# Optimization experiments

Measured on AMD Instinct MI355X. Metric: run time of the kernel, lower is better.

## Reference

```python
import jax, jax.numpy as jnp
import numpy as np

# Config (matches init_kwargs): GRU decoder, score_model='default',
# local_att='False', context_vector_concat='True'. Dropout layers are
# identity (Keras eager call defaults to training=False).
B, L, FEAT = 256, 64, 2048   # batch, attention locations, feature channels
UNITS, EMB, VOCAB = 512, 256, 32000


def setup_inputs() -> dict:
    key = jax.random.key(0)
    ks = jax.random.split(key, 16)
    s = 0.02
    inp = {
        "x_tokens": jax.random.randint(ks[0], (B, 1), 0, VOCAB),
        "features": jax.random.normal(ks[1], (B, L, FEAT), jnp.float32),
        "hidden": jax.random.normal(ks[2], (B, UNITS), jnp.float32),
        # attention params
        "W1": jax.random.normal(ks[3], (FEAT, UNITS), jnp.float32) * s,
        "b1": jnp.zeros((UNITS,), jnp.float32),
        "W2": jax.random.normal(ks[4], (UNITS, UNITS), jnp.float32) * s,
        "b2": jnp.zeros((UNITS,), jnp.float32),
        "V": jax.random.normal(ks[5], (UNITS, 1), jnp.float32) * s,
        "bV": jnp.zeros((1,), jnp.float32),
        "W3": jax.random.normal(ks[6], (FEAT + UNITS, UNITS), jnp.float32) * s,
        "b3": jnp.zeros((UNITS,), jnp.float32),
        # embedding
        "emb_table": jax.random.normal(ks[7], (VOCAB, EMB), jnp.float32) * s,
        # GRU params (gate order z, r, h), input dim = UNITS + EMB
        "gru_kernel": jax.random.normal(ks[8], (UNITS + EMB, 3 * UNITS), jnp.float32) * s,
        "gru_rec": jax.random.normal(ks[9], (UNITS, 3 * UNITS), jnp.float32) * s,
        "gru_bias": jnp.zeros((3 * UNITS,), jnp.float32),
        # output heads
        "fc1_W": jax.random.normal(ks[10], (UNITS, UNITS), jnp.float32) * s,
        "fc1_b": jnp.zeros((UNITS,), jnp.float32),
        "fc2_W": jax.random.normal(ks[11], (UNITS, VOCAB), jnp.float32) * s,
        "fc2_b": jnp.zeros((VOCAB,), jnp.float32),
    }
    return inp


def _gru_step(x_t, h_prev, kernel, rec, bias):
    # Keras GRU single step (reset_after=False), gate order z, r, h.
    u = UNITS
    gx = x_t @ kernel + bias                       # [B, 3u]
    gh = h_prev @ rec                              # [B, 3u]
    z = jax.nn.sigmoid(gx[:, :u] + gh[:, :u])
    r = jax.nn.sigmoid(gx[:, u:2 * u] + gh[:, u:2 * u])
    hh = jnp.tanh(gx[:, 2 * u:] + r * gh[:, 2 * u:])
    return z * h_prev + (1.0 - z) * hh


def reference(x_tokens, features, hidden, W1, b1, W2, b2, V, bV, W3, b3,
              emb_table, gru_kernel, gru_rec, gru_bias,
              fc1_W, fc1_b, fc2_W, fc2_b):
    # Bahdanau attention, score_model='default'
    score = jnp.tanh(features @ W1 + b1 + (hidden @ W2 + b2)[:, None, :])  # [B,L,U]
    logits = score @ V + bV                                               # [B,L,1]
    attn = jax.nn.softmax(logits, axis=1)                                 # [B,L,1]
    context = jnp.sum(attn * features, axis=1)                            # [B,FEAT]
    # context_vector_concat == 'True'
    cvh = jnp.tanh(jnp.concatenate([context, hidden], axis=-1)) @ W3 + b3  # [B,U]
    # embedding + concat with context (seq len 1)
    emb = emb_table[x_tokens]                                             # [B,1,E]
    x_in = jnp.concatenate([cvh[:, None, :], emb], axis=-1)               # [B,1,U+E]
    # GRU over length-1 sequence; Keras Sequential uses zero initial state
    h0 = jnp.zeros((x_in.shape[0], UNITS), x_in.dtype)
    h_new = _gru_step(x_in[:, 0, :], h0, gru_kernel, gru_rec, gru_bias)   # [B,U]
    out = h_new[:, None, :]                                               # [B,1,U]
    x1 = out @ fc1_W + fc1_b                                              # [B,1,U]
    x1 = x1.reshape(-1, x1.shape[2])                                      # [B,U]
    logits_out = x1 @ fc2_W + fc2_b                                       # [B,VOCAB]
    return logits_out, h_new, attn
```

## Files before the change

kernel.cpp:

```cpp
#include <hip/hip_runtime.h>
#include <hip/hip_bf16.h>

#define B_N 256
#define L_Q 64
#define FEAT_N 2048
#define UNITS_N 512
#define EMB_N 256
#define VOCAB_N 32000

typedef __attribute__((ext_vector_type(8))) short bf16x8;
typedef __attribute__((ext_vector_type(4))) float f32x4;

__device__ __forceinline__ unsigned short f2bf(float x) {
  union { float f; unsigned int u; } c; c.f = x;
  unsigned int u = c.u + 0x7FFFu + ((c.u >> 16) & 1u);
  return (unsigned short)(u >> 16);
}

__device__ __forceinline__ float sigmoidf_(float x) { return 1.0f / (1.0f + __expf(-x)); }

__device__ __forceinline__ void store_frag4(unsigned short* base, int KS, int row, int k0,
                                            float a, float b, float c, float d) {
  int rt = row >> 4, lr = row & 15;
  int ks = k0 >> 5, lq = (k0 >> 3) & 3, j0 = k0 & 7;
  union { unsigned long long u; unsigned short s[4]; } p;
  p.s[0] = f2bf(a); p.s[1] = f2bf(b); p.s[2] = f2bf(c); p.s[3] = f2bf(d);
  *reinterpret_cast<unsigned long long*>(base + (((rt * KS + ks) * 64) + (lq * 16 + lr)) * 8 + j0) = p.u;
}

__device__ __forceinline__ void gload_lds16(const void* g, void* lds) {
  __builtin_amdgcn_global_load_lds(
      (const __attribute__((address_space(1))) unsigned int*)(uintptr_t)g,
      (__attribute__((address_space(3))) unsigned int*)(unsigned)(uintptr_t)lds,
      16, 0, 0);
}

__device__ __forceinline__ void wfrag_one(const float* __restrict__ W, int N, int KS,
                                          unsigned short* __restrict__ dst, int tid, int gruMap) {
  int l = tid & 63;
  int ks = (tid >> 6) % KS;
  int cts = tid / (64 * KS);
  int ct = cts & 3, nt = cts >> 2;
  int nb = gruMap ? (nt < 8 ? nt * 64 : 1024 + (nt - 8) * 64) : nt * 64;
  int ncol = nb + ct * 16 + (l & 15);
  int k0 = ks * 32 + (l >> 4) * 8;
  union { bf16x8 v; unsigned short s[8]; } fr;
#pragma unroll
  for (int j = 0; j < 8; ++j) fr.s[j] = f2bf(W[(size_t)(k0 + j) * N + ncol]);
  *reinterpret_cast<bf16x8*>(dst + (size_t)tid * 8) = fr.v;
}

__global__ void k_prep_all(const float* __restrict__ W1, unsigned short* __restrict__ W1s,
                           const float* __restrict__ hidden,
                           const float* __restrict__ emb_table,
                           const int* __restrict__ tok,
                           unsigned short* __restrict__ hfrag,
                           unsigned short* __restrict__ xinfrag,
                           const float* __restrict__ W2, unsigned short* __restrict__ W2f,
                           const float* __restrict__ W3, unsigned short* __restrict__ W3f,
                           const float* __restrict__ gruK, unsigned short* __restrict__ gruf,
                           const float* __restrict__ fc1W, unsigned short* __restrict__ fc1f) {
  int bb = blockIdx.x;
  if (bb < 512) {
    int t = bb * 256 + threadIdx.x;
    int l = t & 63;
    int c = (t >> 6) & 31;
    int kt = t >> 11;
    int n = c * 16 + (l & 15);
    int k0 = kt * 32 + (l >> 4) * 8;
    union { bf16x8 v; unsigned short s[8]; } fr;
#pragma unroll
    for (int j = 0; j < 8; ++j) fr.s[j] = f2bf(W1[(size_t)(k0 + j) * UNITS_N + n]);
    *reinterpret_cast<bf16x8*>(W1s + (size_t)t * 8) = fr.v;
  } else if (bb < 704) {
    int t = (bb - 512) * 256 + threadIdx.x;
    if (t < 32768) {
      int b = t >> 7, k0 = (t & 127) * 4;
      const float* s = hidden + (size_t)b * UNITS_N + k0;
      store_frag4(hfrag, 16, b, k0, s[0], s[1], s[2], s[3]);
    } else if (t < 49152) {
      int t2 = t - 32768;
      int b = t2 >> 6, e0 = (t2 & 63) * 4;
      const float* s = emb_table + (size_t)tok[b] * EMB_N + e0;
      store_frag4(xinfrag, 24, b, 512 + e0, s[0], s[1], s[2], s[3]);
    }
  } else if (bb < 832) {
    wfrag_one(W2, 512, 16, W2f, (bb - 704) * 256 + threadIdx.x, 0);
  } else if (bb < 1472) {
    wfrag_one(W3, 512, 80, W3f, (bb - 832) * 256 + threadIdx.x, 0);
  } else if (bb < 1856) {
    wfrag_one(gruK, 1536, 24, gruf, (bb - 1472) * 256 + threadIdx.x, 1);
  } else {
    wfrag_one(fc1W, 512, 16, fc1f, (bb - 1856) * 256 + threadIdx.x, 0);
  }
}

template <int MODE>
__launch_bounds__(256)
__global__ void k_small2(const unsigned short* __restrict__ Afrag, int KS,
                         const unsigned short* __restrict__ Bfrag,
                         const float* __restrict__ bias,
                         float* __restrict__ outF, int N,
                         unsigned short* __restrict__ outFrag, int KSo) {
  constexpr int NCT = (MODE == 2) ? 8 : 4;
  __shared__ f32x4 red[4][2][NCT][64];
  int t = threadIdx.x, w = t >> 6, l = t & 63;
  int nt = blockIdx.x;
  int mb = blockIdx.y;
  int KSq = KS >> 2;

  f32x4 acc[2][NCT];
#pragma unroll
  for (int rt = 0; rt < 2; ++rt)
#pragma unroll
    for (int ct = 0; ct < NCT; ++ct) acc[rt][ct] = (f32x4){0.f, 0.f, 0.f, 0.f};

  for (int s = 0; s < KSq; ++s) {
    int ks = w * KSq + s;
    bf16x8 af[2];
#pragma unroll
    for (int rt = 0; rt < 2; ++rt)
      af[rt] = *reinterpret_cast<const bf16x8*>(Afrag + (((size_t)(mb * 2 + rt) * KS + ks) * 64 + l) * 8);
#pragma unroll
    for (int ct = 0; ct < NCT; ++ct) {
      int tile = (MODE == 2) ? (ct < 4 ? nt : 8 + nt) : nt;
      int cts = ct & 3;
      bf16x8 bf = *reinterpret_cast<const bf16x8*>(Bfrag + (((size_t)(tile * 4 + cts) * KS + ks) * 64 + l) * 8);
#pragma unroll
      for (int rt = 0; rt < 2; ++rt)
        acc[rt][ct] = __builtin_amdgcn_mfma_f32_16x16x32_bf16(af[rt], bf, acc[rt][ct], 0, 0, 0);
    }
  }

#pragma unroll
  for (int rt = 0; rt < 2; ++rt)
#pragma unroll
    for (int ct = 0; ct < NCT; ++ct) red[w][rt][ct][l] = acc[rt][ct];
  __syncthreads();

#pragma unroll
  for (int si = 0; si < 2; ++si) {
    int s = t + si * 256;
    int l2 = s & 63, ct = (s >> 6) & 3, rt = s >> 8;
    f32x4 v = red[0][rt][ct][l2];
#pragma unroll
    for (int ww = 1; ww < 4; ++ww) v += red[ww][rt][ct][l2];
    int col = nt * 64 + ct * 16 + (l2 & 15);
    int row0 = mb * 32 + rt * 16 + (l2 >> 4) * 4;
    if (MODE == 2) {
      f32x4 vh = red[0][rt][ct + 4][l2];
#pragma unroll
      for (int ww = 1; ww < 4; ++ww) vh += red[ww][rt][ct + 4][l2];
      float bz = bias[col], bh = bias[1024 + col];
#pragma unroll
      for (int i = 0; i < 4; ++i) {
        float hv = (1.f - sigmoidf_(v[i] + bz)) * tanhf(vh[i] + bh);
        int row = row0 + i;
        outF[(size_t)row * UNITS_N + col] = hv;
        int k = col;
        outFrag[(((size_t)(row >> 4) * KSo + (k >> 5)) * 64 + (((k >> 3) & 3) * 16 + (row & 15))) * 8 + (k & 7)] = f2bf(hv);
      }
    } else {
      float bv = bias[col];
#pragma unroll
      for (int i = 0; i < 4; ++i) {
        float vv = v[i] + bv;
        int row = row0 + i;
        if (MODE == 0) {
          outF[(size_t)row * N + col] = vv;
        } else {
          int k = col;
          outFrag[(((size_t)(row >> 4) * KSo + (k >> 5)) * 64 + (((k >> 3) & 3) * 16 + (row & 15))) * 8 + (k & 7)] = f2bf(vv);
        }
      }
    }
  }
}


#define G7_LOADA(S0, S1, KF)                                       \
  { const float* p_ = Ap + (size_t)(KF) * 32;                      \
    S0 = *reinterpret_cast<const float4*>(p_);                     \
    S1 = *reinterpret_cast<const float4*>(p_ + 4); }

#define G7_STAGEB(KF, BUF)                                                          \
  { _Pragma("unroll")                                                               \
    for (int i_ = 0; i_ < 4; ++i_) {                                                \
      int s_ = w * 4 + i_;                                                          \
      gload_lds16(W1c + ((size_t)((KF) * 32 + h * 16 + s_) << 10) + (size_t)l * 16, \
                  BbC + (size_t)(BUF) * 16384 + (s_ << 10));                        \
    } }

#define G7_CONVA(S0, S1, BUF)                                      \
  { union { bf16x8 v; unsigned short s8[8]; } u_;                  \
    u_.s8[0] = f2bf(S0.x); u_.s8[1] = f2bf(S0.y);                  \
    u_.s8[2] = f2bf(S0.z); u_.s8[3] = f2bf(S0.w);                  \
    u_.s8[4] = f2bf(S1.x); u_.s8[5] = f2bf(S1.y);                  \
    u_.s8[6] = f2bf(S1.z); u_.s8[7] = f2bf(S1.w);                  \
    *reinterpret_cast<bf16x8*>(&Ab[BUF][awi]) = u_.v; }

#define G7_BODY(KT, L0, L1, C0, C1)                                           \
  { const int kt_ = (KT);                                                     \
    if (kt_ + 2 < 64) G7_LOADA(L0, L1, kt_ + 2);                              \
    if (kt_ + 1 < 64) {                                                       \
      G7_STAGEB(kt_ + 1, (kt_ + 1) & 1);                                      \
      G7_CONVA(C0, C1, (kt_ + 1) & 1);                                        \
    }                                                                         \
    bf16x8 af_[4];                                                            \
    _Pragma("unroll")                                                         \
    for (int rt_ = 0; rt_ < 4; ++rt_)                                         \
      af_[rt_] = *reinterpret_cast<const bf16x8*>(                            \
          &Ab[kt_ & 1][((rt_ * 4 + (l >> 4)) * 16 + (l & 15)) * 8]);          \
    _Pragma("unroll")                                                         \
    for (int ct_ = 0; ct_ < 4; ++ct_) {                                       \
      bf16x8 bfr_ = *reinterpret_cast<const bf16x8*>(                         \
          &Bb[kt_ & 1][((w * 4 + ct_) * 64 + l) * 8]);                        \
      _Pragma("unroll")                                                       \
      for (int rt_ = 0; rt_ < 4; ++rt_)                                       \
        acc[rt_][ct_] = __builtin_amdgcn_mfma_f32_16x16x32_bf16(              \
            af_[rt_], bfr_, acc[rt_][ct_], 0, 0, 0);                          \
    }                                                                         \
    __syncthreads();                                                          \
  }

__launch_bounds__(256, 2)
__global__ void k_gemm1p(const float* __restrict__ features,
                         const unsigned short* __restrict__ W1s,
                         const float* __restrict__ hproj,
                         const float* __restrict__ b1,
                         const float* __restrict__ V,
                         float* __restrict__ partials) {
  __shared__ unsigned short Bb[2][8192];
  __shared__ unsigned short Ab[2][2048];
  __shared__ float wlog[4][64];

  int t = threadIdx.x, w = t >> 6, l = t & 63;
  int bid = blockIdx.x;
  int swz = (bid & 7) * 64 + (bid >> 3);
  int h = swz & 1;
  int mb = swz >> 1;

  f32x4 acc[4][4];
#pragma unroll
  for (int rt = 0; rt < 4; ++rt)
#pragma unroll
    for (int ct = 0; ct < 4; ++ct) acc[rt][ct] = (f32x4){0.f, 0.f, 0.f, 0.f};

  int r = t >> 2, q = t & 3;
  const float* Ap = features + (size_t)(mb * 64 + r) * FEAT_N + q * 8;
  const int awi = (((r >> 4) * 4 + q) * 16 + (r & 15)) * 8;
  const char* W1c = (const char*)W1s;
  char* BbC = (char*)Bb;

  float4 a00, a01, a10, a11;

  G7_LOADA(a00, a01, 0);
  G7_LOADA(a10, a11, 1);
  G7_STAGEB(0, 0);
  G7_CONVA(a00, a01, 0);
  __syncthreads();

  for (int kt2 = 0; kt2 < 64; kt2 += 2) {
    G7_BODY(kt2,     a00, a01, a10, a11);
    G7_BODY(kt2 + 1, a10, a11, a00, a01);
  }

  float rowpart[16];
#pragma unroll
  for (int i = 0; i < 16; ++i) rowpart[i] = 0.f;
#pragma unroll
  for (int ct = 0; ct < 4; ++ct) {
    int col = h * 256 + w * 64 + ct * 16 + (l & 15);
    float hb = hproj[(size_t)mb * UNITS_N + col] + b1[col];
    float vv = V[col];
#pragma unroll
    for (int rt = 0; rt < 4; ++rt)
#pragma unroll
      for (int i = 0; i < 4; ++i)
        rowpart[rt * 4 + i] += tanhf(acc[rt][ct][i] + hb) * vv;
  }
#pragma unroll
  for (int m = 1; m <= 8; m <<= 1)
#pragma unroll
    for (int i = 0; i < 16; ++i) rowpart[i] += __shfl_xor(rowpart[i], m, 64);
  if ((l & 15) == 0) {
    int g = l >> 4;
#pragma unroll
    for (int rt = 0; rt < 4; ++rt)
#pragma unroll
      for (int i = 0; i < 4; ++i)
        wlog[w][rt * 16 + g * 4 + i] = rowpart[rt * 4 + i];
  }
  __syncthreads();
  if (t < 64) {
    float x = wlog[0][t] + wlog[1][t] + wlog[2][t] + wlog[3][t];
    partials[h * 16384 + mb * 64 + t] = x;
  }
}

__global__ void k_context(const float* __restrict__ features,
                          const float* __restrict__ partials,
                          const float* __restrict__ hidden,
                          unsigned short* __restrict__ tcfrag,
                          float* __restrict__ attn_out) {
  __shared__ float aL[2][64];
  int t = threadIdx.x;
  int half = t >> 9, tt = t & 511;
  int b = blockIdx.x * 2 + half;
  if (tt < 64) {
    float x = partials[b * 64 + tt] + partials[16384 + b * 64 + tt];
    float mx = x;
#pragma unroll
    for (int m = 1; m < 64; m <<= 1) mx = fmaxf(mx, __shfl_xor(mx, m, 64));
    float e = __expf(x - mx);
    float s = e;
#pragma unroll
    for (int m = 1; m < 64; m <<= 1) s += __shfl_xor(s, m, 64);
    float a = e / s;
    aL[half][tt] = a;
    attn_out[(size_t)b * 64 + tt] = a;
  }
  __syncthreads();
  const float* F = features + (size_t)b * 64 * FEAT_N + tt * 4;
  float a0 = 0.f, a1 = 0.f, a2 = 0.f, a3 = 0.f;
#pragma unroll 4
  for (int lr = 0; lr < 64; ++lr) {
    float4 f = *reinterpret_cast<const float4*>(F + (size_t)lr * FEAT_N);
    float av = aL[half][lr];
    a0 += av * f.x; a1 += av * f.y; a2 += av * f.z; a3 += av * f.w;
  }
  store_frag4(tcfrag, 80, b, tt * 4, tanhf(a0), tanhf(a1), tanhf(a2), tanhf(a3));
  if (tt < 128) {
    const float* H = hidden + (size_t)b * UNITS_N + tt * 4;
    store_frag4(tcfrag, 80, b, 2048 + tt * 4, tanhf(H[0]), tanhf(H[1]), tanhf(H[2]), tanhf(H[3]));
  }
}

__launch_bounds__(256)
__global__ void k_fc2(const unsigned short* __restrict__ x1frag,
                      const float* __restrict__ W, const float* __restrict__ bias,
                      float* __restrict__ out) {
  __shared__ unsigned short Bb[4 * 64 * 8];
  int t = threadIdx.x, w = t >> 6, l = t & 63;
  int n0 = blockIdx.x * 64;
  int mh = blockIdx.y;
  f32x4 acc[2][4];
#pragma unroll
  for (int r = 0; r < 2; ++r)
#pragma unroll
    for (int c = 0; c < 4; ++c) acc[r][c] = (f32x4){0.f, 0.f, 0.f, 0.f};

  int sn = t & 63, kc = t >> 6;
  unsigned short* wdst = &Bb[(((sn >> 4) * 64) + ((sn & 15) | (kc << 4))) * 8];
  const float* Wp = W + n0 + sn;
  float wreg[8];
#pragma unroll
  for (int j = 0; j < 8; ++j) wreg[j] = Wp[(size_t)(kc * 8 + j) * VOCAB_N];

  for (int kt = 0; kt < 16; ++kt) {
    __syncthreads();
    {
      union { bf16x8 v; unsigned short s[8]; } p;
#pragma unroll
      for (int j = 0; j < 8; ++j) p.s[j] = f2bf(wreg[j]);
      *reinterpret_cast<bf16x8*>(wdst) = p.v;
    }
    __syncthreads();
    if (kt < 15) {
#pragma unroll
      for (int j = 0; j < 8; ++j) wreg[j] = Wp[(size_t)((kt + 1) * 32 + kc * 8 + j) * VOCAB_N];
    }
    bf16x8 bf[4];
#pragma unroll
    for (int c = 0; c < 4; ++c) bf[c] = *reinterpret_cast<const bf16x8*>(&Bb[((c * 64) + l) * 8]);
#pragma unroll
    for (int rti = 0; rti < 2; ++rti) {
      int rtg = mh * 8 + w * 2 + rti;
      bf16x8 af = *reinterpret_cast<const bf16x8*>(x1frag + ((size_t)(rtg * 16 + kt) * 64 + l) * 8);
#pragma unroll
      for (int c = 0; c < 4; ++c)
        acc[rti][c] = __builtin_amdgcn_mfma_f32_16x16x32_bf16(af, bf[c], acc[rti][c], 0, 0, 0);
    }
  }
#pragma unroll
  for (int c = 0; c < 4; ++c) {
    int col = n0 + c * 16 + (l & 15);
    float bv = bias[col];
#pragma unroll
    for (int rti = 0; rti < 2; ++rti)
#pragma unroll
      for (int i = 0; i < 4; ++i) {
        int row = mh * 128 + w * 32 + rti * 16 + (l >> 4) * 4 + i;
        out[(size_t)row * VOCAB_N + col] = acc[rti][c][i] + bv;
      }
  }
}

extern "C" void kernel_launch(void* const* d_in, const int* in_sizes, int n_in,
                              void* d_out, int out_size, void* d_ws, size_t ws_size,
                              hipStream_t stream) {
  const int*   tok        = (const int*)d_in[0];
  const float* features   = (const float*)d_in[1];
  const float* hidden     = (const float*)d_in[2];
  const float* W1         = (const float*)d_in[3];
  const float* b1         = (const float*)d_in[4];
  const float* W2         = (const float*)d_in[5];
  const float* b2         = (const float*)d_in[6];
  const float* V          = (const float*)d_in[7];
  const float* W3         = (const float*)d_in[9];
  const float* b3         = (const float*)d_in[10];
  const float* emb_table  = (const float*)d_in[11];
  const float* gru_kernel = (const float*)d_in[12];
  const float* gru_bias   = (const float*)d_in[14];
  const float* fc1_W      = (const float*)d_in[15];
  const float* fc1_b      = (const float*)d_in[16];
  const float* fc2_W      = (const float*)d_in[17];
  const float* fc2_b      = (const float*)d_in[18];

  float* out_logits = (float*)d_out;
  float* out_h      = out_logits + (size_t)B_N * VOCAB_N;
  float* out_attn   = out_h + (size_t)B_N * UNITS_N;

  char* ws = (char*)d_ws;
  unsigned short* W1s     = (unsigned short*)(ws);
  float*          hproj   = (float*)(ws + 2097152);
  unsigned short* hfrag   = (unsigned short*)(ws + 2621440);
  unsigned short* tcfrag  = (unsigned short*)(ws + 2883584);
  unsigned short* xinfrag = (unsigned short*)(ws + 4194304);
  unsigned short* hnfrag  = (unsigned short*)(ws + 4587520);
  unsigned short* x1frag  = (unsigned short*)(ws + 4849664);
  float*          partials= (float*)(ws + 5111808);
  unsigned short* W2f     = (unsigned short*)(ws + 5242880);
  unsigned short* W3f     = (unsigned short*)(ws + 5767168);
  unsigned short* gruf    = (unsigned short*)(ws + 8388608);
  unsigned short* fc1f    = (unsigned short*)(ws + 9961472);

  k_prep_all<<<dim3(1984), dim3(256), 0, stream>>>(W1, W1s, hidden, emb_table, tok,
                                                   hfrag, xinfrag, W2, W2f, W3, W3f,
                                                   gru_kernel, gruf, fc1_W, fc1f);
  k_small2<0><<<dim3(8, 8), dim3(256), 0, stream>>>(hfrag, 16, W2f, b2, hproj, 512,
                                                    (unsigned short*)nullptr, 0);
  k_gemm1p<<<dim3(512), dim3(256), 0, stream>>>(features, W1s, hproj, b1, V, partials);
  k_context<<<dim3(128), dim3(1024), 0, stream>>>(features, partials, hidden, tcfrag, out_attn);
  k_small2<1><<<dim3(8, 8), dim3(256), 0, stream>>>(tcfrag, 80, W3f, b3, (float*)nullptr, 0,
                                                    xinfrag, 24);
  k_small2<2><<<dim3(8, 8), dim3(256), 0, stream>>>(xinfrag, 24, gruf, gru_bias, out_h, 512,
                                                    hnfrag, 16);
  k_small2<1><<<dim3(8, 8), dim3(256), 0, stream>>>(hnfrag, 16, fc1f, fc1_b, (float*)nullptr, 0,
                                                    x1frag, 16);
  k_fc2<<<dim3(500, 2), dim3(256), 0, stream>>>(x1frag, fc2_W, fc2_b, out_logits);
}
```

Measured before the change: 141.0 us.

## Enlarge attention GEMM tile to 128 rows with 512-thread blocks

```diff
diff --git a/kernel.cpp b/kernel.cpp
--- a/kernel.cpp
+++ b/kernel.cpp
@@ -15,6 +15,11 @@
   union { float f; unsigned int u; } c; c.f = x;
   unsigned int u = c.u + 0x7FFFu + ((c.u >> 16) & 1u);
   return (unsigned short)(u >> 16);
+}
+
+__device__ __forceinline__ unsigned int pack2bf(float a, float b) {
+  union { float f; unsigned int u; } x, y; x.f = a; y.f = b;
+  return ((y.u + 0x8000u) & 0xFFFF0000u) | ((x.u + 0x8000u) >> 16);
 }
 
 __device__ __forceinline__ float sigmoidf_(float x) { return 1.0f / (1.0f + __expf(-x)); }
@@ -178,43 +183,39 @@
 }
 
 
-#define G7_LOADA(S0, S1, KF)                                       \
-  { const float* p_ = Ap + (size_t)(KF) * 32;                      \
-    S0 = *reinterpret_cast<const float4*>(p_);                     \
-    S1 = *reinterpret_cast<const float4*>(p_ + 4); }
-
-#define G7_STAGEB(KF, BUF)                                                          \
-  { _Pragma("unroll")                                                               \
-    for (int i_ = 0; i_ < 4; ++i_) {                                                \
-      int s_ = w * 4 + i_;                                                          \
-      gload_lds16(W1c + ((size_t)((KF) * 32 + h * 16 + s_) << 10) + (size_t)l * 16, \
-                  BbC + (size_t)(BUF) * 16384 + (s_ << 10));                        \
-    } }
-
-#define G7_CONVA(S0, S1, BUF)                                      \
-  { union { bf16x8 v; unsigned short s8[8]; } u_;                  \
-    u_.s8[0] = f2bf(S0.x); u_.s8[1] = f2bf(S0.y);                  \
-    u_.s8[2] = f2bf(S0.z); u_.s8[3] = f2bf(S0.w);                  \
-    u_.s8[4] = f2bf(S1.x); u_.s8[5] = f2bf(S1.y);                  \
-    u_.s8[6] = f2bf(S1.z); u_.s8[7] = f2bf(S1.w);                  \
-    *reinterpret_cast<bf16x8*>(&Ab[BUF][awi]) = u_.v; }
-
-#define G7_BODY(KT, L0, L1, C0, C1)                                           \
+#define GM_LOADA(S, KF)                                            \
+  { const float* p_ = Ap0 + (size_t)(KF) * 32;                     \
+    S[0] = *reinterpret_cast<const float4*>(p_);                   \
+    S[1] = *reinterpret_cast<const float4*>(p_ + 4); }
+
+#define GM_STAGEB(KT, BUF)                                                         \
+  { gload_lds16(gB0 + (size_t)(KT) * 16384, BbC + (BUF) * 16384 + bd0);            \
+    gload_lds16(gB0 + (size_t)(KT) * 16384 + 4096, BbC + (BUF) * 16384 + bd0 + 8192); }
+
+#define GM_CONVA(S, BUF)                                           \
+  { union { bf16x8 v; unsigned int u4[4]; } d_;                    \
+    d_.u4[0] = pack2bf(S[0].x, S[0].y);                            \
+    d_.u4[1] = pack2bf(S[0].z, S[0].w);                            \
+    d_.u4[2] = pack2bf(S[1].x, S[1].y);                            \
+    d_.u4[3] = pack2bf(S[1].z, S[1].w);                            \
+    *reinterpret_cast<bf16x8*>(&Ab[BUF][awi]) = d_.v; }
+
+#define GM_BODY(KT, LS, CS)                                                   \
   { const int kt_ = (KT);                                                     \
-    if (kt_ + 2 < 64) G7_LOADA(L0, L1, kt_ + 2);                              \
+    if (kt_ + 2 < 64) GM_LOADA(LS, kt_ + 2);                                  \
     if (kt_ + 1 < 64) {                                                       \
-      G7_STAGEB(kt_ + 1, (kt_ + 1) & 1);                                      \
-      G7_CONVA(C0, C1, (kt_ + 1) & 1);                                        \
+      GM_STAGEB(kt_ + 1, (kt_ + 1) & 1);                                      \
+      GM_CONVA(CS, (kt_ + 1) & 1);                                            \
     }                                                                         \
     bf16x8 af_[4];                                                            \
     _Pragma("unroll")                                                         \
     for (int rt_ = 0; rt_ < 4; ++rt_)                                         \
       af_[rt_] = *reinterpret_cast<const bf16x8*>(                            \
-          &Ab[kt_ & 1][((rt_ * 4 + (l >> 4)) * 16 + (l & 15)) * 8]);          \
+          &Ab[kt_ & 1][((wr * 4 + rt_) * 64 + l) * 8]);                       \
     _Pragma("unroll")                                                         \
     for (int ct_ = 0; ct_ < 4; ++ct_) {                                       \
       bf16x8 bfr_ = *reinterpret_cast<const bf16x8*>(                         \
-          &Bb[kt_ & 1][((w * 4 + ct_) * 64 + l) * 8]);                        \
+          &Bb[kt_ & 1][((wc * 4 + ct_) * 64 + l) * 8]);                       \
       _Pragma("unroll")                                                       \
       for (int rt_ = 0; rt_ < 4; ++rt_)                                       \
         acc[rt_][ct_] = __builtin_amdgcn_mfma_f32_16x16x32_bf16(              \
@@ -223,22 +224,23 @@
     __syncthreads();                                                          \
   }
 
-__launch_bounds__(256, 2)
-__global__ void k_gemm1p(const float* __restrict__ features,
+__launch_bounds__(512, 1)
+__global__ void k_gemm1m(const float* __restrict__ features,
                          const unsigned short* __restrict__ W1s,
                          const float* __restrict__ hproj,
                          const float* __restrict__ b1,
                          const float* __restrict__ V,
                          float* __restrict__ partials) {
+  __shared__ unsigned short Ab[2][4096];
   __shared__ unsigned short Bb[2][8192];
-  __shared__ unsigned short Ab[2][2048];
-  __shared__ float wlog[4][64];
+  __shared__ float wlog[8][64];
 
   int t = threadIdx.x, w = t >> 6, l = t & 63;
+  int wr = w >> 2, wc = w & 3;
   int bid = blockIdx.x;
-  int swz = (bid & 7) * 64 + (bid >> 3);
-  int h = swz & 1;
-  int mb = swz >> 1;
+  int swz = (bid & 7) * 32 + (bid >> 3);
+  int nh = swz & 1;
+  int mh = swz >> 1;
 
   f32x4 acc[4][4];
 #pragma unroll
@@ -247,31 +249,33 @@
     for (int ct = 0; ct < 4; ++ct) acc[rt][ct] = (f32x4){0.f, 0.f, 0.f, 0.f};
 
   int r = t >> 2, q = t & 3;
-  const float* Ap = features + (size_t)(mb * 64 + r) * FEAT_N + q * 8;
-  const int awi = (((r >> 4) * 4 + q) * 16 + (r & 15)) * 8;
-  const char* W1c = (const char*)W1s;
+  const float* Ap0 = features + (size_t)(mh * 128 + r) * FEAT_N + q * 8;
+  const int awi = (((r >> 4) * 64) + q * 16 + (r & 15)) * 8;
+  const unsigned short* gB0 = W1s + ((size_t)(nh * 16 + (t >> 6)) * 64 + (t & 63)) * 8;
+  const int bd0 = (((t >> 6) * 64) + (t & 63)) * 16;
   char* BbC = (char*)Bb;
 
-  float4 a00, a01, a10, a11;
-
-  G7_LOADA(a00, a01, 0);
-  G7_LOADA(a10, a11, 1);
-  G7_STAGEB(0, 0);
-  G7_CONVA(a00, a01, 0);
+  float4 aS[2], bS[2];
+
+  GM_LOADA(aS, 0);
+  GM_LOADA(bS, 1);
+  GM_STAGEB(0, 0);
+  GM_CONVA(aS, 0);
   __syncthreads();
 
   for (int kt2 = 0; kt2 < 64; kt2 += 2) {
-    G7_BODY(kt2,     a00, a01, a10, a11);
-    G7_BODY(kt2 + 1, a10, a11, a00, a01);
-  }
-
+    GM_BODY(kt2, aS, bS);
+    GM_BODY(kt2 + 1, bS, aS);
+  }
+
+  int bw = mh * 2 + wr;
   float rowpart[16];
 #pragma unroll
   for (int i = 0; i < 16; ++i) rowpart[i] = 0.f;
 #pragma unroll
   for (int ct = 0; ct < 4; ++ct) {
-    int col = h * 256 + w * 64 + ct * 16 + (l & 15);
-    float hb = hproj[(size_t)mb * UNITS_N + col] + b1[col];
+    int col = nh * 256 + wc * 64 + ct * 16 + (l & 15);
+    float hb = hproj[(size_t)bw * UNITS_N + col] + b1[col];
     float vv = V[col];
 #pragma unroll
     for (int rt = 0; rt < 4; ++rt)
@@ -292,9 +296,12 @@
         wlog[w][rt * 16 + g * 4 + i] = rowpart[rt * 4 + i];
   }
   __syncthreads();
-  if (t < 64) {
-    float x = wlog[0][t] + wlog[1][t] + wlog[2][t] + wlog[3][t];
-    partials[h * 16384 + mb * 64 + t] = x;
+  if (t < 128) {
+    int rr = t;
+    int wrg = rr >> 6;
+    float x = wlog[wrg * 4 + 0][rr & 63] + wlog[wrg * 4 + 1][rr & 63] +
+              wlog[wrg * 4 + 2][rr & 63] + wlog[wrg * 4 + 3][rr & 63];
+    partials[nh * 16384 + mh * 128 + rr] = x;
   }
 }
 
@@ -302,13 +309,14 @@
                           const float* __restrict__ partials,
                           const float* __restrict__ hidden,
                           unsigned short* __restrict__ tcfrag,
-                          float* __restrict__ attn_out) {
+                          float* __restrict__ attn_out, int nsets) {
   __shared__ float aL[2][64];
   int t = threadIdx.x;
   int half = t >> 9, tt = t & 511;
   int b = blockIdx.x * 2 + half;
   if (tt < 64) {
-    float x = partials[b * 64 + tt] + partials[16384 + b * 64 + tt];
+    float x = 0.f;
+    for (int p = 0; p < nsets; ++p) x += partials[p * 16384 + b * 64 + tt];
     float mx = x;
 #pragma unroll
     for (int m = 1; m < 64; m <<= 1) mx = fmaxf(mx, __shfl_xor(mx, m, 64));
@@ -429,19 +437,20 @@
   unsigned short* xinfrag = (unsigned short*)(ws + 4194304);
   unsigned short* hnfrag  = (unsigned short*)(ws + 4587520);
   unsigned short* x1frag  = (unsigned short*)(ws + 4849664);
-  float*          partials= (float*)(ws + 5111808);
   unsigned short* W2f     = (unsigned short*)(ws + 5242880);
   unsigned short* W3f     = (unsigned short*)(ws + 5767168);
   unsigned short* gruf    = (unsigned short*)(ws + 8388608);
   unsigned short* fc1f    = (unsigned short*)(ws + 9961472);
+  float*          partials= (float*)(ws + 10485760);
 
   k_prep_all<<<dim3(1984), dim3(256), 0, stream>>>(W1, W1s, hidden, emb_table, tok,
                                                    hfrag, xinfrag, W2, W2f, W3, W3f,
                                                    gru_kernel, gruf, fc1_W, fc1f);
   k_small2<0><<<dim3(8, 8), dim3(256), 0, stream>>>(hfrag, 16, W2f, b2, hproj, 512,
                                                     (unsigned short*)nullptr, 0);
-  k_gemm1p<<<dim3(512), dim3(256), 0, stream>>>(features, W1s, hproj, b1, V, partials);
-  k_context<<<dim3(128), dim3(1024), 0, stream>>>(features, partials, hidden, tcfrag, out_attn);
+  k_gemm1m<<<dim3(256), dim3(512), 0, stream>>>(features, W1s, hproj, b1, V, partials);
+  k_context<<<dim3(128), dim3(1024), 0, stream>>>(features, partials, hidden, tcfrag,
+                                                  out_attn, 2);
   k_small2<1><<<dim3(8, 8), dim3(256), 0, stream>>>(tcfrag, 80, W3f, b3, (float*)nullptr, 0,
                                                     xinfrag, 24);
   k_small2<2><<<dim3(8, 8), dim3(256), 0, stream>>>(xinfrag, 24, gruf, gru_bias, out_h, 512,
```

New measurement: 156.0 us. 10.6% more time.
